# Kernel tuning notes

Measured on AMD Instinct MI355X. Metric: run time of the kernel, lower is better.

Reference implementation:

```python
import jax, jax.numpy as jnp
import numpy as np

B, T, D = 64, 4096, 512

def setup_inputs() -> dict:
    key = jax.random.key(0)
    k1, k2 = jax.random.split(key)
    encoder_outputs = jax.random.normal(k1, (B, T, D), dtype=jnp.float32)
    attn_weights_param = jax.random.normal(k2, (D, 1), dtype=jnp.float32)
    return {"encoder_outputs": encoder_outputs, "attn_weights_param": attn_weights_param}

def reference(encoder_outputs, attn_weights_param):
    # scores: [B, T] = encoder_outputs @ v  (GEMV per batch)
    energies = jnp.einsum('btd,d->bt', encoder_outputs, attn_weights_param[:, 0])
    weights = jax.nn.softmax(energies, axis=1)                 # [B, T]
    context = jnp.einsum('bt,btd->bd', weights, encoder_outputs)  # weighted-sum pool
    return (context, weights)
```

## Files before the change

### kernel.cpp

```cpp
#include <hip/hip_runtime.h>

constexpr int B = 64;
constexpr int T = 4096;
constexpr int D = 512;
constexpr int CHUNKS = 16;
constexpr int ROWS_PER_CHUNK = T / CHUNKS;
constexpr int PART_STRIDE = D + 2;

__global__ __launch_bounds__(256) void attn_pass1(
    const float* __restrict__ enc,
    const float* __restrict__ v,
    float* __restrict__ energies,
    float* __restrict__ partials)
{
    const int blk   = blockIdx.x;
    const int b     = blk / CHUNKS;
    const int chunk = blk % CHUNKS;
    const int tid   = threadIdx.x;
    const int wave  = tid >> 6;
    const int lane  = tid & 63;

    const float4 v0 = *(const float4*)(v + lane * 4);
    const float4 v1 = *(const float4*)(v + 256 + lane * 4);

    float  m = -3.0e38f;
    float  l = 0.0f;
    float4 o0 = make_float4(0.f, 0.f, 0.f, 0.f);
    float4 o1 = make_float4(0.f, 0.f, 0.f, 0.f);

    const int t0 = chunk * ROWS_PER_CHUNK;
    const float* encb = enc + (size_t)b * T * D;

    for (int k = 0; k < ROWS_PER_CHUNK / 4; ++k) {
        const int t = t0 + wave + 4 * k;
        const float* row = encb + (size_t)t * D;
        const float4 a0 = *(const float4*)(row + lane * 4);
        const float4 a1 = *(const float4*)(row + 256 + lane * 4);

        float e = a0.x * v0.x + a0.y * v0.y + a0.z * v0.z + a0.w * v0.w
                + a1.x * v1.x + a1.y * v1.y + a1.z * v1.z + a1.w * v1.w;
        #pragma unroll
        for (int off = 32; off > 0; off >>= 1)
            e += __shfl_xor(e, off, 64);

        if (lane == 0) energies[(size_t)b * T + t] = e;

        const float m_new = fmaxf(m, e);
        const float corr  = __expf(m - m_new);
        const float p     = __expf(e - m_new);
        l = l * corr + p;
        o0.x = o0.x * corr + p * a0.x;
        o0.y = o0.y * corr + p * a0.y;
        o0.z = o0.z * corr + p * a0.z;
        o0.w = o0.w * corr + p * a0.w;
        o1.x = o1.x * corr + p * a1.x;
        o1.y = o1.y * corr + p * a1.y;
        o1.z = o1.z * corr + p * a1.z;
        o1.w = o1.w * corr + p * a1.w;
        m = m_new;
    }

    __shared__ float sm[4];
    __shared__ float sl[4];
    __shared__ float so[4][D];

    if (lane == 0) { sm[wave] = m; sl[wave] = l; }
    *(float4*)&so[wave][lane * 4]       = o0;
    *(float4*)&so[wave][256 + lane * 4] = o1;
    __syncthreads();

    const float m_blk = fmaxf(fmaxf(sm[0], sm[1]), fmaxf(sm[2], sm[3]));
    const float s0 = __expf(sm[0] - m_blk);
    const float s1 = __expf(sm[1] - m_blk);
    const float s2 = __expf(sm[2] - m_blk);
    const float s3 = __expf(sm[3] - m_blk);
    const float l_blk = sl[0] * s0 + sl[1] * s1 + sl[2] * s2 + sl[3] * s3;

    float* part = partials + (size_t)blk * PART_STRIDE;
    if (tid == 0) { part[0] = m_blk; part[1] = l_blk; }
    for (int d = tid; d < D; d += 256) {
        part[2 + d] = so[0][d] * s0 + so[1][d] * s1
                    + so[2][d] * s2 + so[3][d] * s3;
    }
}

__global__ __launch_bounds__(256) void attn_pass2(
    const float* __restrict__ partials,
    float* __restrict__ ctx,
    float* __restrict__ weights)
{
    const int b   = blockIdx.x;
    const int tid = threadIdx.x;
    const float* pb = partials + (size_t)b * CHUNKS * PART_STRIDE;

    float m_g = -3.0e38f;
    #pragma unroll
    for (int c = 0; c < CHUNKS; ++c)
        m_g = fmaxf(m_g, pb[c * PART_STRIDE]);

    float sc[CHUNKS];
    float l_g = 0.0f;
    #pragma unroll
    for (int c = 0; c < CHUNKS; ++c) {
        const float s = __expf(pb[c * PART_STRIDE] - m_g);
        sc[c] = s;
        l_g += pb[c * PART_STRIDE + 1] * s;
    }
    const float inv_l = 1.0f / l_g;

    for (int d = tid; d < D; d += 256) {
        float acc = 0.0f;
        #pragma unroll
        for (int c = 0; c < CHUNKS; ++c)
            acc += pb[c * PART_STRIDE + 2 + d] * sc[c];
        ctx[(size_t)b * D + d] = acc * inv_l;
    }

    float* wrow = weights + (size_t)b * T;
    for (int t = tid; t < T; t += 256) {
        wrow[t] = __expf(wrow[t] - m_g) * inv_l;
    }
}

extern "C" void kernel_launch(void* const* d_in, const int* in_sizes, int n_in,
                              void* d_out, int out_size, void* d_ws, size_t ws_size,
                              hipStream_t stream) {
    const float* enc = (const float*)d_in[0];
    const float* v   = (const float*)d_in[1];
    float* out     = (float*)d_out;
    float* ctx     = out;
    float* weights = out + B * D;
    float* partials = (float*)d_ws;

    attn_pass1<<<B * CHUNKS, 256, 0, stream>>>(enc, v, weights, partials);
    attn_pass2<<<B, 256, 0, stream>>>(partials, ctx, weights);
}
```

Measured before the change: 683.0 us.

## Process four rows per wave per iteration and split pass2 across four blocks

```diff
diff --git a/kernel.cpp b/kernel.cpp
--- a/kernel.cpp
+++ b/kernel.cpp
@@ -6,6 +6,12 @@
 constexpr int CHUNKS = 16;
 constexpr int ROWS_PER_CHUNK = T / CHUNKS;
 constexpr int PART_STRIDE = D + 2;
+
+__device__ __forceinline__ float dot8(const float4& a0, const float4& v0,
+                                      const float4& a1, const float4& v1) {
+    return a0.x * v0.x + a0.y * v0.y + a0.z * v0.z + a0.w * v0.w
+         + a1.x * v1.x + a1.y * v1.y + a1.z * v1.z + a1.w * v1.w;
+}
 
 __global__ __launch_bounds__(256) void attn_pass1(
     const float* __restrict__ enc,
@@ -31,32 +37,50 @@
     const int t0 = chunk * ROWS_PER_CHUNK;
     const float* encb = enc + (size_t)b * T * D;
 
-    for (int k = 0; k < ROWS_PER_CHUNK / 4; ++k) {
-        const int t = t0 + wave + 4 * k;
+    for (int k = 0; k < ROWS_PER_CHUNK / 16; ++k) {
+        const int t = t0 + k * 16 + wave * 4;
         const float* row = encb + (size_t)t * D;
-        const float4 a0 = *(const float4*)(row + lane * 4);
-        const float4 a1 = *(const float4*)(row + 256 + lane * 4);
 
-        float e = a0.x * v0.x + a0.y * v0.y + a0.z * v0.z + a0.w * v0.w
-                + a1.x * v1.x + a1.y * v1.y + a1.z * v1.z + a1.w * v1.w;
+        float4 a0[4], a1[4];
         #pragma unroll
-        for (int off = 32; off > 0; off >>= 1)
-            e += __shfl_xor(e, off, 64);
+        for (int r = 0; r < 4; ++r) {
+            a0[r] = *(const float4*)(row + r * D + lane * 4);
+            a1[r] = *(const float4*)(row + r * D + 256 + lane * 4);
+        }
 
-        if (lane == 0) energies[(size_t)b * T + t] = e;
+        float e[4];
+        #pragma unroll
+        for (int r = 0; r < 4; ++r)
+            e[r] = dot8(a0[r], v0, a1[r], v1);
 
-        const float m_new = fmaxf(m, e);
-        const float corr  = __expf(m - m_new);
-        const float p     = __expf(e - m_new);
-        l = l * corr + p;
-        o0.x = o0.x * corr + p * a0.x;
-        o0.y = o0.y * corr + p * a0.y;
-        o0.z = o0.z * corr + p * a0.z;
-        o0.w = o0.w * corr + p * a0.w;
-        o1.x = o1.x * corr + p * a1.x;
-        o1.y = o1.y * corr + p * a1.y;
-        o1.z = o1.z * corr + p * a1.z;
-        o1.w = o1.w * corr + p * a1.w;
+        #pragma unroll
+        for (int off = 32; off > 0; off >>= 1) {
+            #pragma unroll
+            for (int r = 0; r < 4; ++r)
+                e[r] += __shfl_xor(e[r], off, 64);
+        }
+
+        if (lane == 0)
+            *(float4*)(energies + (size_t)b * T + t) =
+                make_float4(e[0], e[1], e[2], e[3]);
+
+        float m_new = m;
+        #pragma unroll
+        for (int r = 0; r < 4; ++r) m_new = fmaxf(m_new, e[r]);
+        const float corr = __expf(m - m_new);
+        float p[4];
+        #pragma unroll
+        for (int r = 0; r < 4; ++r) p[r] = __expf(e[r] - m_new);
+        l = l * corr + p[0] + p[1] + p[2] + p[3];
+
+        o0.x = o0.x * corr + p[0]*a0[0].x + p[1]*a0[1].x + p[2]*a0[2].x + p[3]*a0[3].x;
+        o0.y = o0.y * corr + p[0]*a0[0].y + p[1]*a0[1].y + p[2]*a0[2].y + p[3]*a0[3].y;
+        o0.z = o0.z * corr + p[0]*a0[0].z + p[1]*a0[1].z + p[2]*a0[2].z + p[3]*a0[3].z;
+        o0.w = o0.w * corr + p[0]*a0[0].w + p[1]*a0[1].w + p[2]*a0[2].w + p[3]*a0[3].w;
+        o1.x = o1.x * corr + p[0]*a1[0].x + p[1]*a1[1].x + p[2]*a1[2].x + p[3]*a1[3].x;
+        o1.y = o1.y * corr + p[0]*a1[0].y + p[1]*a1[1].y + p[2]*a1[2].y + p[3]*a1[3].y;
+        o1.z = o1.z * corr + p[0]*a1[0].z + p[1]*a1[1].z + p[2]*a1[2].z + p[3]*a1[3].z;
+        o1.w = o1.w * corr + p[0]*a1[0].w + p[1]*a1[1].w + p[2]*a1[2].w + p[3]*a1[3].w;
         m = m_new;
     }
 
@@ -89,8 +113,9 @@
     float* __restrict__ ctx,
     float* __restrict__ weights)
 {
-    const int b   = blockIdx.x;
-    const int tid = threadIdx.x;
+    const int b     = blockIdx.x >> 2;
+    const int slice = blockIdx.x & 3;
+    const int tid   = threadIdx.x;
     const float* pb = partials + (size_t)b * CHUNKS * PART_STRIDE;
 
     float m_g = -3.0e38f;
@@ -108,18 +133,23 @@
     }
     const float inv_l = 1.0f / l_g;
 
-    for (int d = tid; d < D; d += 256) {
-        float acc = 0.0f;
-        #pragma unroll
-        for (int c = 0; c < CHUNKS; ++c)
-            acc += pb[c * PART_STRIDE + 2 + d] * sc[c];
-        ctx[(size_t)b * D + d] = acc * inv_l;
+    if (slice == 0) {
+        for (int d = tid; d < D; d += 256) {
+            float acc = 0.0f;
+            #pragma unroll
+            for (int c = 0; c < CHUNKS; ++c)
+                acc += pb[c * PART_STRIDE + 2 + d] * sc[c];
+            ctx[(size_t)b * D + d] = acc * inv_l;
+        }
     }
 
-    float* wrow = weights + (size_t)b * T;
-    for (int t = tid; t < T; t += 256) {
-        wrow[t] = __expf(wrow[t] - m_g) * inv_l;
-    }
+    float* wrow = weights + (size_t)b * T + slice * (T / 4);
+    float4 w = *(float4*)(wrow + tid * 4);
+    w.x = __expf(w.x - m_g) * inv_l;
+    w.y = __expf(w.y - m_g) * inv_l;
+    w.z = __expf(w.z - m_g) * inv_l;
+    w.w = __expf(w.w - m_g) * inv_l;
+    *(float4*)(wrow + tid * 4) = w;
 }
 
 extern "C" void kernel_launch(void* const* d_in, const int* in_sizes, int n_in,
@@ -133,5 +163,5 @@
     float* partials = (float*)d_ws;
 
     attn_pass1<<<B * CHUNKS, 256, 0, stream>>>(enc, v, weights, partials);
-    attn_pass2<<<B, 256, 0, stream>>>(partials, ctx, weights);
+    attn_pass2<<<B * 4, 256, 0, stream>>>(partials, ctx, weights);
 }
```

Measured after the change: 682.9 us. About the same (-0.0%).
